# Kernel tuning notes

Hardware: AMD Instinct MI355X
Metric: run time of the kernel (lower is better)

Reference implementation:

```python
import jax, jax.numpy as jnp
from jax import lax
import numpy as np

B, DIM, HEADS, L, K = 8, 128, 8, 4096, 3
INNER = DIM * HEADS
PAD = K // 2
EPS = 1e-5
SCALE = DIM ** -0.5


def setup_inputs() -> dict:
    key = jax.random.key(0)
    ks = jax.random.split(key, 32)

    def n(i, shape, s):
        return jax.random.normal(ks[i], shape, jnp.float32) * s

    inp = {"x": jax.random.normal(ks[0], (B, DIM, L), jnp.float32)}
    inp["ln1_g"] = jnp.ones((DIM,), jnp.float32)
    inp["ln1_b"] = jnp.zeros((DIM,), jnp.float32)
    for idx, p in enumerate(("q", "k", "v")):
        base = 1 + idx * 2
        inp[p + "_dw"] = n(base, (DIM, 1, K), 0.2)        # depthwise kernel
        inp[p + "_bn_g"] = jnp.ones((DIM,), jnp.float32)
        inp[p + "_bn_b"] = jnp.zeros((DIM,), jnp.float32)
        inp[p + "_bn_m"] = jnp.zeros((DIM,), jnp.float32)  # running mean
        inp[p + "_bn_v"] = jnp.ones((DIM,), jnp.float32)   # running var
        inp[p + "_pw"] = n(base + 1, (INNER, DIM), 0.05)   # 1x1 conv dim->inner
    inp["dwc_dw"] = n(8, (DIM,), 0.2)                      # kernel-1 depthwise = per-channel scale
    inp["dwc_bn_g"] = jnp.ones((DIM,), jnp.float32)
    inp["dwc_bn_b"] = jnp.zeros((DIM,), jnp.float32)
    inp["dwc_bn_m"] = jnp.zeros((DIM,), jnp.float32)
    inp["dwc_bn_v"] = jnp.ones((DIM,), jnp.float32)
    inp["dwc_pw"] = n(9, (DIM, DIM), 0.05)
    inp["out_w"] = n(10, (DIM, INNER), 0.05)
    inp["out_b"] = jnp.zeros((DIM,), jnp.float32)
    inp["ln2_g"] = jnp.ones((DIM,), jnp.float32)
    inp["ln2_b"] = jnp.zeros((DIM,), jnp.float32)
    inp["ff_w1"] = n(11, (4 * DIM, DIM), 0.05)
    inp["ff_b1"] = jnp.zeros((4 * DIM,), jnp.float32)
    inp["ff_w2"] = n(12, (DIM, 4 * DIM), 0.05)
    inp["ff_b2"] = jnp.zeros((DIM,), jnp.float32)
    return inp


def _layernorm(x, g, b):
    # channel-wise LN over axis=1 (unbiased=False variance)
    m = jnp.mean(x, axis=1, keepdims=True)
    v = jnp.var(x, axis=1, keepdims=True)
    return (x - m) / jnp.sqrt(v + EPS) * g[None, :, None] + b[None, :, None]


def _dw_block(x, dw, g, b, m, v, pw):
    # depthwise conv (k=K, same padding) -> eval-mode BN -> 1x1 conv
    y = lax.conv_general_dilated(x, dw, (1,), [(PAD, PAD)],
                                 feature_group_count=DIM,
                                 dimension_numbers=("NCH", "OIH", "NCH"))
    y = (y - m[None, :, None]) * (g / jnp.sqrt(v + EPS))[None, :, None] + b[None, :, None]
    return jnp.einsum("oi,bil->bol", pw, y)


def reference(x, ln1_g, ln1_b,
              q_dw, q_bn_g, q_bn_b, q_bn_m, q_bn_v, q_pw,
              k_dw, k_bn_g, k_bn_b, k_bn_m, k_bn_v, k_pw,
              v_dw, v_bn_g, v_bn_b, v_bn_m, v_bn_v, v_pw,
              dwc_dw, dwc_bn_g, dwc_bn_b, dwc_bn_m, dwc_bn_v, dwc_pw,
              out_w, out_b, ln2_g, ln2_b, ff_w1, ff_b1, ff_w2, ff_b2):
    # ---- attention block (PreNorm + residual) ----
    xn = _layernorm(x, ln1_g, ln1_b)
    q = _dw_block(xn, q_dw, q_bn_g, q_bn_b, q_bn_m, q_bn_v, q_pw)  # [B, INNER, L]
    k = _dw_block(xn, k_dw, k_bn_g, k_bn_b, k_bn_m, k_bn_v, k_pw)
    v = _dw_block(xn, v_dw, v_bn_g, v_bn_b, v_bn_m, v_bn_v, v_pw)

    def split(t):  # b (h d) x -> (b h) x d
        return t.reshape(B, HEADS, DIM, L).transpose(0, 1, 3, 2).reshape(B * HEADS, L, DIM)

    q, k, v = split(q), split(k), split(v)
    k_soft = jax.nn.softmax(k, axis=-1)                       # softmax over feature dim d
    kk = jnp.einsum("nxd,nxe->nde", q, k_soft) * SCALE        # [(bh), d, d]
    # DWConv gate on q (kernel-1 depthwise -> BN -> 1x1), channels = DIM
    g_ = q * dwc_dw[None, None, :]
    g_ = (g_ - dwc_bn_m) * (dwc_bn_g / jnp.sqrt(dwc_bn_v + EPS)) + dwc_bn_b
    g_ = jnp.einsum("od,nxd->nxo", dwc_pw, g_)
    gate = jax.nn.sigmoid(g_) * v
    out = jnp.einsum("nxd,nde->nxe", v, kk) + gate            # [(bh), L, d]
    out = out.reshape(B, HEADS, L, DIM).transpose(0, 1, 3, 2).reshape(B, INNER, L)
    attn = jnp.einsum("oi,bil->bol", out_w, out) + out_b[None, :, None]
    x = attn + x

    # ---- feed-forward block (PreNorm + residual) ----
    xn = _layernorm(x, ln2_g, ln2_b)
    h = jnp.einsum("oi,bil->bol", ff_w1, xn) + ff_b1[None, :, None]
    h = jax.nn.gelu(h, approximate=False)
    h = jnp.einsum("oi,bil->bol", ff_w2, h) + ff_b2[None, :, None]
    return h + x
```

## Files before the change

kernel.cpp:

```cpp
#include <hip/hip_runtime.h>
#include <hip/hip_bf16.h>
#include <math.h>

#define DI __device__ __forceinline__

namespace {

constexpr int L = 4096;
constexpr float EPS = 1e-5f;
constexpr float SCALEF = 0.08838834764831845f;

typedef unsigned short u16;
typedef unsigned int u32;
typedef unsigned char u8;
typedef __attribute__((ext_vector_type(8))) short bf16x8;
typedef __attribute__((ext_vector_type(4))) float f32x4;

DI float b2f(u16 h){ u32 u = ((u32)h) << 16; float f; __builtin_memcpy(&f, &u, 4); return f; }
DI u16 f2b(float f){ u32 u; __builtin_memcpy(&u, &f, 4); u32 r = u + 0x7fffu + ((u >> 16) & 1u); return (u16)(r >> 16); }
DI float sigmoidf(float x){ return 1.f / (1.f + __expf(-x)); }

DI uint2 pack_fp8x8(const float* v){
  u32 lo = __builtin_amdgcn_cvt_pk_fp8_f32(v[0], v[1], 0, false);
  lo = (u32)__builtin_amdgcn_cvt_pk_fp8_f32(v[2], v[3], lo, true);
  u32 hi = __builtin_amdgcn_cvt_pk_fp8_f32(v[4], v[5], 0, false);
  hi = (u32)__builtin_amdgcn_cvt_pk_fp8_f32(v[6], v[7], hi, true);
  return make_uint2(lo, hi);
}
DI u8 f2e(float v){ return (u8)__builtin_amdgcn_cvt_pk_fp8_f32(v, v, 0, false); }
DI float e2f(u8 c){ return __builtin_amdgcn_cvt_f32_fp8((int)c, 0); }

DI int boff(int o, int d8){ return ((o >> 4) << 11) + (d8 << 7) + (((o & 15) ^ d8) << 3); }
DI int foff(int g, int k8, int nn){ return (g << 11) + (k8 << 7) + (nn << 3); }
DI int faddr(int x, int e){ return ((x >> 4) << 11) + ((e >> 3) << 7) + ((x & 15) << 3) + (e & 7); }
DI int t8off(int dhi, int nl, int x8){ return (dhi << 11) + (x8 << 7) + (((nl ^ x8 ^ dhi) & 15) << 3); }

DI void stage_a(const u16* __restrict__ g, int rs, u16* a_s, int tid){
  #pragma unroll
  for (int it = 0; it < 4; it++){
    int item = tid + 256 * it;
    int d8 = item & 15, l = item >> 4;
    *(uint4*)&a_s[l * 136 + d8 * 8] = *(const uint4*)&g[(size_t)l * rs + d8 * 8];
  }
}

__global__ __launch_bounds__(256) void ln_kernel(
    const float* __restrict__ x, const float* __restrict__ g,
    const float* __restrict__ bt, u16* __restrict__ o)
{
  const int tid = threadIdx.x;
  const int pos = blockIdx.x * 64 + (tid >> 2);
  const int part = tid & 3;
  const int b = pos >> 12, l = pos & (L - 1);
  const float* xb = x + (size_t)b * 128 * L + l;
  float vv[32];
  float s = 0.f, ss = 0.f;
  #pragma unroll
  for (int i = 0; i < 32; i++){
    float v = xb[(size_t)(part * 32 + i) * L];
    vv[i] = v; s += v; ss += v * v;
  }
  s += __shfl_xor(s, 1);  s += __shfl_xor(s, 2);
  ss += __shfl_xor(ss, 1); ss += __shfl_xor(ss, 2);
  const float m = s * (1.f / 128.f);
  const float rs = rsqrtf(ss * (1.f / 128.f) - m * m + EPS);
  #pragma unroll
  for (int c = 0; c < 4; c++){
    u16 pk[8];
    #pragma unroll
    for (int j = 0; j < 8; j++){
      int d = part * 32 + c * 8 + j;
      pk[j] = f2b((vv[c * 8 + j] - m) * rs * g[d] + bt[d]);
    }
    uint4 uu; __builtin_memcpy(&uu, pk, 16);
    *(uint4*)&o[(size_t)pos * 128 + part * 32 + c * 8] = uu;
  }
}

__global__ __launch_bounds__(256) void wpack_kernel(
    const float* __restrict__ q_pw, const float* __restrict__ k_pw,
    const float* __restrict__ v_pw, const float* __restrict__ out_w,
    const float* __restrict__ ff_w1, const float* __restrict__ ff_w2,
    const float* __restrict__ dwc_dw, const float* __restrict__ dwc_bng,
    const float* __restrict__ dwc_bnv, const float* __restrict__ dwc_bnb,
    const float* __restrict__ dwc_bnm, const float* __restrict__ dwc_pw,
    u16* __restrict__ wpk, float* __restrict__ c2, u8* __restrict__ wpk8)
{
  const int blk = blockIdx.x;
  const int tid = threadIdx.x;
  if (blk < 37){
    int t8 = blk;
    #pragma unroll
    for (int it = 0; it < 8; it++){
      int item = tid + 256 * it;
      int nn = item & 15, k8 = (item >> 4) & 15, os = item >> 8;
      int o = os * 16 + nn;
      float fv[8];
      if (t8 < 24){
        int p = t8 >> 3, h = t8 & 7;
        const float* pw = (p == 0) ? q_pw : (p == 1 ? k_pw : v_pw);
        #pragma unroll
        for (int j = 0; j < 8; j++)
          fv[j] = pw[(size_t)(h * 128 + o) * 128 + k8 * 8 + j] * 16.f;
      } else if (t8 < 32){
        #pragma unroll
        for (int j = 0; j < 8; j++)
          fv[j] = out_w[(size_t)o * 1024 + (t8 - 24) * 128 + k8 * 8 + j] * 16.f;
      } else if (t8 < 36){
        #pragma unroll
        for (int j = 0; j < 8; j++)
          fv[j] = ff_w1[(size_t)((t8 - 32) * 128 + o) * 128 + k8 * 8 + j] * 16.f;
      } else {
        #pragma unroll
        for (int j = 0; j < 8; j++){
          int d = k8 * 8 + j;
          float sD = dwc_bng[d] * rsqrtf(dwc_bnv[d] + EPS);
          fv[j] = dwc_pw[(size_t)o * 128 + d] * dwc_dw[d] * sD * 16.f;
        }
      }
      *(uint2*)&wpk8[(size_t)t8 * 16384 + foff(os, k8, nn)] = pack_fp8x8(fv);
    }
  } else if (blk < 69){
    int vitem = (blk - 37) * 256 + tid;
    int d8 = vitem & 15;
    int o  = (vitem >> 4) & 127;
    int t  = 36 + (vitem >> 11);
    const float* src = ff_w2 + (size_t)o * 512 + (t - 36) * 128 + d8 * 8;
    u16 pk[8];
    #pragma unroll
    for (int j = 0; j < 8; j++) pk[j] = f2b(src[j]);
    uint4 uu; __builtin_memcpy(&uu, pk, 16);
    *(uint4*)&wpk[(size_t)t * 16384 + boff(o, d8)] = uu;
  } else {
    int e = tid;
    if (e < 128){
      float cacc = 0.f;
      for (int d = 0; d < 128; d++){
        float sD = dwc_bng[d] * rsqrtf(dwc_bnv[d] + EPS);
        cacc += dwc_pw[(size_t)e * 128 + d] * (dwc_bnb[d] - dwc_bnm[d] * sD);
      }
      c2[e] = cacc;
    }
  }
}

struct QkvArgs {
  const float* dw[3];
  const float* bng[3];
  const float* bnb[3];
  const float* bnm[3];
  const float* bnv[3];
  u8* outp[3];
};

__global__ __launch_bounds__(256, 5) void qkv_fused_kernel(
    const u16* __restrict__ xnb, const u8* __restrict__ wpk8, QkvArgs args)
{
  __shared__ __attribute__((aligned(16))) u8 y_s8[64 * 136];
  __shared__ u16 st_s[64 * 136];
  __shared__ float4 coef[128];
  const int tid = threadIdx.x;
  const int lb = blockIdx.x;
  const int oh = blockIdx.y;
  const int bz = blockIdx.z;
  const int b  = bz / 3;
  const int p  = bz % 3;
  const int l0 = lb * 64;
  const int lane = tid & 63, wv = tid >> 6;
  const int nn = lane & 15, quad = lane >> 4;
  const int d8s = tid & 15;
  u8* w_s8 = (u8*)st_s;

  if (tid < 128){
    int d = tid;
    float sD = args.bng[p][d] * rsqrtf(args.bnv[p][d] + EPS);
    const float* dw = args.dw[p];
    coef[d] = make_float4(dw[d * 3] * sD, dw[d * 3 + 1] * sD, dw[d * 3 + 2] * sD,
                          args.bnb[p][d] - args.bnm[p][d] * sD);
  }
  __syncthreads();
  float4 cf[8];
  #pragma unroll
  for (int jj = 0; jj < 8; jj++) cf[jj] = coef[d8s * 8 + jj];
  #pragma unroll
  for (int it = 0; it < 4; it++){
    int l = (tid >> 4) + it * 16;
    int gl = l0 + l;
    const u16* rowp = xnb + ((size_t)b * L + gl) * 128 + d8s * 8;
    uint4 uc = *(const uint4*)rowp;
    uint4 um = (gl > 0)     ? *(const uint4*)(rowp - 128) : make_uint4(0, 0, 0, 0);
    uint4 up = (gl < L - 1) ? *(const uint4*)(rowp + 128) : make_uint4(0, 0, 0, 0);
    u16 em[8], ec[8], ep[8];
    __builtin_memcpy(em, &um, 16); __builtin_memcpy(ec, &uc, 16); __builtin_memcpy(ep, &up, 16);
    float fv[8];
    #pragma unroll
    for (int jj = 0; jj < 8; jj++)
      fv[jj] = cf[jj].x * b2f(em[jj]) + cf[jj].y * b2f(ec[jj]) + cf[jj].z * b2f(ep[jj]) + cf[jj].w;
    *(uint2*)&y_s8[l * 136 + d8s * 8] = pack_fp8x8(fv);
  }
  __syncthreads();
  long afq[4];
  #pragma unroll
  for (int dc = 0; dc < 4; dc++)
    afq[dc] = *(const long*)&y_s8[(wv * 16 + nn) * 136 + ((dc << 2) + quad) * 8];

  for (int hh = 0; hh < 4; hh++){
    const int h = oh * 4 + hh;
    if (hh) __syncthreads();
    const u8* src = wpk8 + ((size_t)(p * 8 + h) << 14);
    #pragma unroll
    for (int it = 0; it < 4; it++){
      int idx = (tid + 256 * it) << 4;
      *(uint4*)&w_s8[idx] = *(const uint4*)&src[idx];
    }
    __syncthreads();
    f32x4 acc[8];
    #pragma unroll
    for (int os = 0; os < 8; os++) acc[os] = (f32x4){0.f, 0.f, 0.f, 0.f};
    #pragma unroll
    for (int os = 0; os < 8; os++){
      #pragma unroll
      for (int dc = 0; dc < 4; dc++){
        int d8 = (dc << 2) + quad;
        long bf8 = *(const long*)&w_s8[foff(os, d8, nn)];
        acc[os] = __builtin_amdgcn_mfma_f32_16x16x32_fp8_fp8(afq[dc], bf8, acc[os], 0, 0, 0);
      }
    }
    #pragma unroll
    for (int os = 0; os < 8; os++)
      #pragma unroll
      for (int r = 0; r < 4; r++) acc[os][r] *= 0.0625f;
    if (p == 1){
      #pragma unroll
      for (int r = 0; r < 4; r++){
        float m = acc[0][r];
        #pragma unroll
        for (int os = 1; os < 8; os++) m = fmaxf(m, acc[os][r]);
        m = fmaxf(m, __shfl_xor(m, 1));
        m = fmaxf(m, __shfl_xor(m, 2));
        m = fmaxf(m, __shfl_xor(m, 4));
        m = fmaxf(m, __shfl_xor(m, 8));
        float s = 0.f;
        #pragma unroll
        for (int os = 0; os < 8; os++){ acc[os][r] = __expf(acc[os][r] - m); s += acc[os][r]; }
        s += __shfl_xor(s, 1);
        s += __shfl_xor(s, 2);
        s += __shfl_xor(s, 4);
        s += __shfl_xor(s, 8);
        float inv = 16.f / s;
        #pragma unroll
        for (int os = 0; os < 8; os++) acc[os][r] *= inv;
      }
    }
    __syncthreads();
    #pragma unroll
    for (int os = 0; os < 8; os++)
      #pragma unroll
      for (int r = 0; r < 4; r++)
        st_s[(wv * 16 + quad * 4 + r) * 136 + (os << 4) + nn] = f2b(acc[os][r]);
    __syncthreads();
    if (p == 2){
      u8* v8 = args.outp[2];
      size_t tbase = ((size_t)((b * 8 + h) * 64 + lb)) << 13;
      #pragma unroll
      for (int it = 0; it < 4; it++){
        int g = it, e8 = tid >> 4, n2 = tid & 15;
        const u16* sp = &st_s[(g * 16 + n2) * 136 + e8 * 8];
        float fv[8];
        #pragma unroll
        for (int j = 0; j < 8; j++) fv[j] = b2f(sp[j]);
        *(uint2*)&v8[tbase + foff(g, e8, n2)] = pack_fp8x8(fv);
      }
    } else {
      u8* outp8 = args.outp[p];
      size_t gbase = ((size_t)(b * 8 + h) * L + l0) * 128;
      #pragma unroll
      for (int it = 0; it < 4; it++){
        int item = tid + 256 * it;
        int row = item >> 4, d8 = item & 15;
        const u16* sp = &st_s[row * 136 + d8 * 8];
        float fv[8];
        #pragma unroll
        for (int j = 0; j < 8; j++) fv[j] = b2f(sp[j]);
        *(uint2*)&outp8[gbase + (size_t)row * 128 + d8 * 8] = pack_fp8x8(fv);
      }
    }
  }
}

__global__ __launch_bounds__(256, 3) void kk_kernel(
    const u8* __restrict__ qt8, const u8* __restrict__ kt8,
    float* __restrict__ kkp)
{
  __shared__ u8 qT8[16384];
  __shared__ u8 kT8[16384];
  const int tid = threadIdx.x;
  const int sp = blockIdx.x;
  const int n  = blockIdx.y;
  const int d8 = tid & 15;
  const int x8 = tid >> 4;
  const int lane = tid & 63, wv = tid >> 6;
  const int nn = lane & 15, quad = lane >> 4;
  const int m4 = (wv >> 1) << 2;
  const int e4 = (wv & 1) << 2;
  const size_t gbase = ((size_t)n * L + sp * 1024) * 128;

  uint2 rq[8], rk[8];
  #pragma unroll
  for (int j = 0; j < 8; j++){
    size_t off = gbase + (size_t)(x8 * 8 + j) * 128 + d8 * 8;
    rq[j] = *(const uint2*)&qt8[off];
    rk[j] = *(const uint2*)&kt8[off];
  }

  f32x4 acc[4][4];
  #pragma unroll
  for (int mi = 0; mi < 4; mi++)
    #pragma unroll
    for (int ei = 0; ei < 4; ei++) acc[mi][ei] = (f32x4){0.f, 0.f, 0.f, 0.f};

  for (int c = 0; c < 8; c++){
    #pragma unroll
    for (int i = 0; i < 8; i++){
      u8 cq[8], ck[8];
      #pragma unroll
      for (int j = 0; j < 8; j++){
        u8 tmp[8];
        __builtin_memcpy(tmp, &rq[j], 8); cq[j] = tmp[i];
        __builtin_memcpy(tmp, &rk[j], 8); ck[j] = tmp[i];
      }
      int d = d8 * 8 + i;
      int off = t8off(d >> 4, d & 15, x8);
      uint2 uq, uk;
      __builtin_memcpy(&uq, cq, 8); __builtin_memcpy(&uk, ck, 8);
      *(uint2*)&qT8[off] = uq;
      *(uint2*)&kT8[off] = uk;
    }
    __syncthreads();
    if (c < 7){
      #pragma unroll
      for (int j = 0; j < 8; j++){
        size_t off = gbase + (size_t)((c + 1) * 128 + x8 * 8 + j) * 128 + d8 * 8;
        rq[j] = *(const uint2*)&qt8[off];
        rk[j] = *(const uint2*)&kt8[off];
      }
    }
    #pragma unroll
    for (int ks = 0; ks < 4; ks++){
      int x8f = (ks << 2) + quad;
      long af[4], bf[4];
      #pragma unroll
      for (int t = 0; t < 4; t++){
        af[t] = *(const long*)&qT8[t8off(m4 + t, nn, x8f)];
        bf[t] = *(const long*)&kT8[t8off(e4 + t, nn, x8f)];
      }
      #pragma unroll
      for (int mi = 0; mi < 4; mi++)
        #pragma unroll
        for (int ei = 0; ei < 4; ei++)
          acc[mi][ei] = __builtin_amdgcn_mfma_f32_16x16x32_fp8_fp8(af[mi], bf[ei], acc[mi][ei], 0, 0, 0);
    }
    __syncthreads();
  }

  float* op = kkp + ((size_t)(sp * 64 + n) << 14);
  #pragma unroll
  for (int mi = 0; mi < 4; mi++){
    #pragma unroll
    for (int r = 0; r < 4; r++){
      int d = (m4 << 4) + mi * 16 + quad * 4 + r;
      #pragma unroll
      for (int ei = 0; ei < 4; ei++)
        op[d * 128 + (e4 << 4) + ei * 16 + nn] = acc[mi][ei][r];
    }
  }
}

__global__ __launch_bounds__(256) void kkred_kernel(
    const float* __restrict__ kkp, u8* __restrict__ kkbb8)
{
  int item = blockIdx.x * 256 + threadIdx.x;
  int nn = item & 15, d8 = (item >> 4) & 15, os = (item >> 8) & 7, n = item >> 11;
  int e = os * 16 + nn;
  float fv[8];
  #pragma unroll
  for (int j = 0; j < 8; j++){
    float s = 0.f;
    #pragma unroll
    for (int sp = 0; sp < 4; sp++)
      s += kkp[(size_t)sp * (64 * 16384) + n * 16384 + (d8 * 8 + j) * 128 + e];
    fv[j] = s * (SCALEF * 2.f);
  }
  *(uint2*)&kkbb8[((size_t)n << 14) + foff(os, d8, nn)] = pack_fp8x8(fv);
}

__global__ __launch_bounds__(256, 4) void gateout_kernel(
    const u8* __restrict__ qt8, const u8* __restrict__ vt8,
    const u8* __restrict__ kkbb8, const u8* __restrict__ w2tb8,
    const float* __restrict__ c2, u8* __restrict__ outt8)
{
  __shared__ __attribute__((aligned(16))) u8 q_s8[64 * 144];
  __shared__ __attribute__((aligned(16))) u8 v_s8[8192];
  const int tid = threadIdx.x;
  const int lb = blockIdx.x;
  const int n  = blockIdx.y;
  const int l0 = lb * 64;
  const int lane = tid & 63, wv = tid >> 6;
  const int nn = lane & 15, quad = lane >> 4;
  const size_t vtile = ((size_t)(n * 64 + lb)) << 13;
  const size_t qbase = ((size_t)n * L + l0) * 128;

  #pragma unroll
  for (int it = 0; it < 4; it++){
    int item = tid + 256 * it;
    int d8b = item & 15, l = item >> 4;
    *(uint2*)&q_s8[l * 144 + d8b * 8] = *(const uint2*)&qt8[qbase + (size_t)l * 128 + d8b * 8];
  }
  #pragma unroll
  for (int it = 0; it < 2; it++){
    int idx = (tid + 256 * it) << 4;
    *(uint4*)&v_s8[idx] = *(const uint4*)&vt8[vtile + idx];
  }
  __syncthreads();

  long aq[4], av[4];
  #pragma unroll
  for (int dc = 0; dc < 4; dc++){
    aq[dc] = *(const long*)&q_s8[(wv * 16 + nn) * 144 + ((dc << 2) + quad) * 8];
    av[dc] = *(const long*)&v_s8[foff(wv, (dc << 2) + quad, nn)];
  }
  const u8* kb8 = kkbb8 + ((size_t)n << 14);
  f32x4 acc_o[8], acc_g[8];
  #pragma unroll
  for (int os = 0; os < 8; os++){ acc_o[os] = (f32x4){0,0,0,0}; acc_g[os] = (f32x4){0,0,0,0}; }
  #pragma unroll
  for (int os = 0; os < 8; os++){
    #pragma unroll
    for (int dc = 0; dc < 4; dc++){
      int d8 = (dc << 2) + quad;
      long bkk = *(const long*)&kb8[foff(os, d8, nn)];
      long bw8 = *(const long*)&w2tb8[foff(os, d8, nn)];
      acc_o[os] = __builtin_amdgcn_mfma_f32_16x16x32_fp8_fp8(av[dc], bkk, acc_o[os], 0, 0, 0);
      acc_g[os] = __builtin_amdgcn_mfma_f32_16x16x32_fp8_fp8(aq[dc], bw8, acc_g[os], 0, 0, 0);
    }
  }
  __syncthreads();
  u8* st8 = q_s8;
  #pragma unroll
  for (int os = 0; os < 8; os++){
    int e = (os << 4) + nn;
    float c2v = c2[e];
    #pragma unroll
    for (int r = 0; r < 4; r++){
      int xr = wv * 16 + quad * 4 + r;
      float ve = e2f(v_s8[faddr(xr, e)]);
      float val = acc_o[os][r] * (1.f / 32.f) + sigmoidf(acc_g[os][r] * 0.0625f + c2v) * ve;
      st8[faddr(xr, e)] = f2e(val);
    }
  }
  __syncthreads();
  #pragma unroll
  for (int it = 0; it < 2; it++){
    int idx = (tid + 256 * it) << 4;
    *(uint4*)&outt8[vtile + idx] = *(const uint4*)&st8[idx];
  }
}

__global__ __launch_bounds__(256, 4) void outw_kernel(
    const u8* __restrict__ outt8, const u8* __restrict__ wpk8o,
    const float* __restrict__ out_b, const float* __restrict__ x,
    const float* __restrict__ g2, const float* __restrict__ bt2,
    float* __restrict__ x2, u8* __restrict__ xn2b8)
{
  __shared__ float stf[128 * 68];
  const int tid = threadIdx.x;
  const int lb = blockIdx.x;
  const int b  = blockIdx.y;
  const int l0 = lb * 64;
  const int lane = tid & 63, wv = tid >> 6;
  const int nn = lane & 15, quad = lane >> 4;
  f32x4 acc[8];
  #pragma unroll
  for (int os = 0; os < 8; os++) acc[os] = (f32x4){0,0,0,0};

  for (int h = 0; h < 8; h++){
    const size_t tbase = ((size_t)((b * 8 + h) * 64 + lb)) << 13;
    long af[4];
    #pragma unroll
    for (int dc = 0; dc < 4; dc++)
      af[dc] = *(const long*)&outt8[tbase + foff(wv, (dc << 2) + quad, nn)];
    const u8* bp8 = wpk8o + (h << 14);
    #pragma unroll
    for (int os = 0; os < 8; os++){
      #pragma unroll
      for (int dc = 0; dc < 4; dc++){
        long bf8 = *(const long*)&bp8[foff(os, (dc << 2) + quad, nn)];
        acc[os] = __builtin_amdgcn_mfma_f32_16x16x32_fp8_fp8(af[dc], bf8, acc[os], 0, 0, 0);
      }
    }
  }
  #pragma unroll
  for (int os = 0; os < 8; os++)
    #pragma unroll
    for (int r = 0; r < 4; r++)
      stf[((os << 4) + nn) * 68 + wv * 16 + quad * 4 + r] = acc[os][r] * 0.0625f;
  __syncthreads();
  {
    int o = tid >> 1, lh = tid & 1;
    float bias = out_b[o];
    size_t gbase = ((size_t)b * 128 + o) * L + l0 + lh * 32;
    float* sp = &stf[o * 68 + lh * 32];
    #pragma unroll
    for (int k = 0; k < 8; k++){
      float4 xv = *(const float4*)&x[gbase + k * 4];
      float4 sv = *(float4*)&sp[k * 4];
      float4 ov = make_float4(sv.x + bias + xv.x, sv.y + bias + xv.y,
                              sv.z + bias + xv.z, sv.w + bias + xv.w);
      *(float4*)&sp[k * 4] = ov;
      *(float4*)&x2[gbase + k * 4] = ov;
    }
  }
  __syncthreads();
  {
    int l = tid >> 2, part = tid & 3;
    float vv[32];
    float s = 0.f, ss = 0.f;
    #pragma unroll
    for (int i = 0; i < 32; i++){
      float v = stf[(part * 32 + i) * 68 + l];
      vv[i] = v; s += v; ss += v * v;
    }
    s += __shfl_xor(s, 1);  s += __shfl_xor(s, 2);
    ss += __shfl_xor(ss, 1); ss += __shfl_xor(ss, 2);
    float m = s * (1.f / 128.f);
    float rs = rsqrtf(ss * (1.f / 128.f) - m * m + EPS);
    #pragma unroll
    for (int c = 0; c < 4; c++){
      float fv[8];
      #pragma unroll
      for (int j = 0; j < 8; j++){
        int d = part * 32 + c * 8 + j;
        fv[j] = (vv[c * 8 + j] - m) * rs * g2[d] + bt2[d];
      }
      *(uint2*)&xn2b8[((size_t)b * L + l0 + l) * 128 + part * 32 + c * 8] = pack_fp8x8(fv);
    }
  }
}

__global__ __launch_bounds__(256, 4) void ff_fused_kernel(
    const u8* __restrict__ xn2b8, const u8* __restrict__ wpk8,
    const u16* __restrict__ wpk,
    const float* __restrict__ b1, const float* __restrict__ b2,
    const float* __restrict__ x2, float* __restrict__ outp)
{
  __shared__ __attribute__((aligned(16))) u8 a_s8[64 * 136];
  __shared__ u16 h_s[64 * 136];
  const int tid = threadIdx.x;
  const int lb = blockIdx.x;
  const int b  = blockIdx.y;
  const int l0 = lb * 64;
  const int lane = tid & 63, wv = tid >> 6;
  const int nn = lane & 15, quad = lane >> 4;

  #pragma unroll
  for (int it = 0; it < 4; it++){
    int item = tid + 256 * it;
    int d8 = item & 15, l = item >> 4;
    *(uint2*)&a_s8[l * 136 + d8 * 8] =
        *(const uint2*)&xn2b8[((size_t)b * L + l0 + l) * 128 + d8 * 8];
  }
  __syncthreads();
  long af8[4];
  #pragma unroll
  for (int dc = 0; dc < 4; dc++)
    af8[dc] = *(const long*)&a_s8[(wv * 16 + nn) * 136 + ((dc << 2) + quad) * 8];

  f32x4 acc_out[8];
  #pragma unroll
  for (int os = 0; os < 8; os++) acc_out[os] = (f32x4){0.f, 0.f, 0.f, 0.f};

  for (int fc = 0; fc < 4; fc++){
    const u8* bp1 = wpk8 + (size_t)(32 + fc) * 16384;
    f32x4 hacc[8];
    #pragma unroll
    for (int os = 0; os < 8; os++) hacc[os] = (f32x4){0.f, 0.f, 0.f, 0.f};
    #pragma unroll
    for (int os = 0; os < 8; os++){
      #pragma unroll
      for (int dc = 0; dc < 4; dc++){
        long bf8 = *(const long*)&bp1[foff(os, (dc << 2) + quad, nn)];
        hacc[os] = __builtin_amdgcn_mfma_f32_16x16x32_fp8_fp8(af8[dc], bf8, hacc[os], 0, 0, 0);
      }
    }
    __syncthreads();
    #pragma unroll
    for (int os = 0; os < 8; os++){
      float bias = b1[fc * 128 + (os << 4) + nn];
      #pragma unroll
      for (int r = 0; r < 4; r++){
        float v = hacc[os][r] * 0.0625f + bias;
        float ge = 0.5f * v * (1.f + erff(v * 0.70710678118654752f));
        h_s[(wv * 16 + quad * 4 + r) * 136 + (os << 4) + nn] = f2b(ge);
      }
    }
    __syncthreads();
    bf16x8 hf[4];
    #pragma unroll
    for (int dc = 0; dc < 4; dc++)
      hf[dc] = *(const bf16x8*)&h_s[(wv * 16 + nn) * 136 + ((dc << 2) + quad) * 8];
    const u16* bp2 = wpk + (size_t)(36 + fc) * 16384;
    #pragma unroll
    for (int os = 0; os < 8; os++){
      #pragma unroll
      for (int dc = 0; dc < 4; dc++){
        int d8 = (dc << 2) + quad;
        bf16x8 bf = *(const bf16x8*)&bp2[(os << 11) + (d8 << 7) + ((nn ^ d8) << 3)];
        acc_out[os] = __builtin_amdgcn_mfma_f32_16x16x32_bf16(hf[dc], bf, acc_out[os], 0, 0, 0);
      }
    }
  }

  float* stf = (float*)h_s;
  #pragma unroll
  for (int t = 0; t < 2; t++){
    __syncthreads();
    #pragma unroll
    for (int osl = 0; osl < 4; osl++){
      int os = t * 4 + osl;
      #pragma unroll
      for (int r = 0; r < 4; r++)
        stf[((osl << 4) + nn) * 68 + wv * 16 + quad * 4 + r] = acc_out[os][r];
    }
    __syncthreads();
    int ol = tid >> 2;
    int o  = t * 64 + ol;
    int lc = (tid & 3) * 16;
    float bias = b2[o];
    size_t gbase = ((size_t)b * 128 + o) * L + l0 + lc;
    #pragma unroll
    for (int k = 0; k < 4; k++){
      float4 sv = *(const float4*)&stf[ol * 68 + lc + k * 4];
      float4 xv = *(const float4*)&x2[gbase + k * 4];
      *(float4*)&outp[gbase + k * 4] = make_float4(sv.x + bias + xv.x, sv.y + bias + xv.y,
                                                   sv.z + bias + xv.z, sv.w + bias + xv.w);
    }
  }
}

}

extern "C" void kernel_launch(void* const* d_in, const int* in_sizes, int n_in,
                              void* d_out, int out_size, void* d_ws, size_t ws_size,
                              hipStream_t stream)
{
  const float* x      = (const float*)d_in[0];
  const float* ln1_g  = (const float*)d_in[1];
  const float* ln1_b  = (const float*)d_in[2];
  const float* q_dw   = (const float*)d_in[3];
  const float* q_bng  = (const float*)d_in[4];
  const float* q_bnb  = (const float*)d_in[5];
  const float* q_bnm  = (const float*)d_in[6];
  const float* q_bnv  = (const float*)d_in[7];
  const float* q_pw   = (const float*)d_in[8];
  const float* k_dw   = (const float*)d_in[9];
  const float* k_bng  = (const float*)d_in[10];
  const float* k_bnb  = (const float*)d_in[11];
  const float* k_bnm  = (const float*)d_in[12];
  const float* k_bnv  = (const float*)d_in[13];
  const float* k_pw   = (const float*)d_in[14];
  const float* v_dw   = (const float*)d_in[15];
  const float* v_bng  = (const float*)d_in[16];
  const float* v_bnb  = (const float*)d_in[17];
  const float* v_bnm  = (const float*)d_in[18];
  const float* v_bnv  = (const float*)d_in[19];
  const float* v_pw   = (const float*)d_in[20];
  const float* dwc_dw  = (const float*)d_in[21];
  const float* dwc_bng = (const float*)d_in[22];
  const float* dwc_bnb = (const float*)d_in[23];
  const float* dwc_bnm = (const float*)d_in[24];
  const float* dwc_bnv = (const float*)d_in[25];
  const float* dwc_pw  = (const float*)d_in[26];
  const float* out_w  = (const float*)d_in[27];
  const float* out_b  = (const float*)d_in[28];
  const float* ln2_g  = (const float*)d_in[29];
  const float* ln2_b  = (const float*)d_in[30];
  const float* ff_w1  = (const float*)d_in[31];
  const float* ff_b1  = (const float*)d_in[32];
  const float* ff_w2  = (const float*)d_in[33];
  const float* ff_b2  = (const float*)d_in[34];
  float* out = (float*)d_out;

  char* w = (char*)d_ws;
  u8*   qt8   = (u8*)(w);
  u8*   kt8   = (u8*)(w + (32ull  << 20));
  u8*   outt8 = (u8*)(w + (64ull  << 20));
  u8*   vt8   = (u8*)(w + (128ull << 20));
  u16*  xnb   = (u16*)(w + (192ull << 20));
  u8*   kkbb8 = (u8*)(w + (192ull << 20));
  u8*   xn2b8 = (u8*)(w + (192ull << 20));
  float* kkp  = (float*)(w + (200ull << 20));
  float* x2   = kkp;
  float* c2   = (float*)(w + (216ull << 20));
  u16*  wpk   = (u16*)(w + (216ull << 20) + 65536);
  u8*   wpk8  = (u8*)(w + (218ull << 20));
  u8*   wpk8o = wpk8 + ((size_t)24 << 14);
  u8*   w2tb8 = wpk8 + ((size_t)36 << 14);

  ln_kernel<<<512, 256, 0, stream>>>(x, ln1_g, ln1_b, xnb);
  wpack_kernel<<<70, 256, 0, stream>>>(q_pw, k_pw, v_pw, out_w, ff_w1, ff_w2,
                                       dwc_dw, dwc_bng, dwc_bnv, dwc_bnb, dwc_bnm, dwc_pw,
                                       wpk, c2, wpk8);

  QkvArgs qa;
  qa.dw[0] = q_dw;  qa.bng[0] = q_bng; qa.bnb[0] = q_bnb; qa.bnm[0] = q_bnm; qa.bnv[0] = q_bnv; qa.outp[0] = qt8;
  qa.dw[1] = k_dw;  qa.bng[1] = k_bng; qa.bnb[1] = k_bnb; qa.bnm[1] = k_bnm; qa.bnv[1] = k_bnv; qa.outp[1] = kt8;
  qa.dw[2] = v_dw;  qa.bng[2] = v_bng; qa.bnb[2] = v_bnb; qa.bnm[2] = v_bnm; qa.bnv[2] = v_bnv; qa.outp[2] = vt8;
  qkv_fused_kernel<<<dim3(64, 2, 24), 256, 0, stream>>>(xnb, wpk8, qa);

  kk_kernel<<<dim3(4, 64), 256, 0, stream>>>(qt8, kt8, kkp);
  kkred_kernel<<<512, 256, 0, stream>>>(kkp, kkbb8);
  gateout_kernel<<<dim3(64, 64), 256, 0, stream>>>(qt8, vt8, kkbb8, w2tb8, c2, outt8);
  outw_kernel<<<dim3(64, 8), 256, 0, stream>>>(outt8, wpk8o, out_b, x, ln2_g, ln2_b, x2, xn2b8);

  ff_fused_kernel<<<dim3(64, 8), 256, 0, stream>>>(xn2b8, wpk8, wpk, ff_b1, ff_b2, x2, out);
}
```

Baseline: 354.8 us.

## Process all heads per QKV block and stage outputs directly as fp8

The QKV kernel now loops over all 8 heads in one block instead of splitting heads across two blocks. This halves the grid and avoids recomputing the depthwise conv and LN-loaded tile twice. The output staging buffer drops from bf16 with a later fp8 repack to fp8 written straight into the reused weight buffer via f2e/faddr, and the value path is copied out with 16-byte copies. Shared memory shrinks, which may raise occupancy, but each block now runs longer over a smaller grid (1536 blocks).

```diff
diff --git a/kernel.cpp b/kernel.cpp
--- a/kernel.cpp
+++ b/kernel.cpp
@@ -157,19 +157,17 @@
     const u16* __restrict__ xnb, const u8* __restrict__ wpk8, QkvArgs args)
 {
   __shared__ __attribute__((aligned(16))) u8 y_s8[64 * 136];
-  __shared__ u16 st_s[64 * 136];
+  __shared__ __attribute__((aligned(16))) u8 w_s8[16384];
   __shared__ float4 coef[128];
   const int tid = threadIdx.x;
   const int lb = blockIdx.x;
-  const int oh = blockIdx.y;
-  const int bz = blockIdx.z;
+  const int bz = blockIdx.y;
   const int b  = bz / 3;
   const int p  = bz % 3;
   const int l0 = lb * 64;
   const int lane = tid & 63, wv = tid >> 6;
   const int nn = lane & 15, quad = lane >> 4;
   const int d8s = tid & 15;
-  u8* w_s8 = (u8*)st_s;
 
   if (tid < 128){
     int d = tid;
@@ -204,9 +202,8 @@
   for (int dc = 0; dc < 4; dc++)
     afq[dc] = *(const long*)&y_s8[(wv * 16 + nn) * 136 + ((dc << 2) + quad) * 8];
 
-  for (int hh = 0; hh < 4; hh++){
-    const int h = oh * 4 + hh;
-    if (hh) __syncthreads();
+  for (int h = 0; h < 8; h++){
+    if (h) __syncthreads();
     const u8* src = wpk8 + ((size_t)(p * 8 + h) << 14);
     #pragma unroll
     for (int it = 0; it < 4; it++){
@@ -253,23 +250,32 @@
       }
     }
     __syncthreads();
-    #pragma unroll
-    for (int os = 0; os < 8; os++)
-      #pragma unroll
-      for (int r = 0; r < 4; r++)
-        st_s[(wv * 16 + quad * 4 + r) * 136 + (os << 4) + nn] = f2b(acc[os][r]);
+    u8* st8 = w_s8;
+    if (p == 2){
+      #pragma unroll
+      for (int os = 0; os < 8; os++){
+        int e = (os << 4) + nn;
+        #pragma unroll
+        for (int r = 0; r < 4; r++)
+          st8[faddr(wv * 16 + quad * 4 + r, e)] = f2e(acc[os][r]);
+      }
+    } else {
+      #pragma unroll
+      for (int os = 0; os < 8; os++){
+        int e = (os << 4) + nn;
+        #pragma unroll
+        for (int r = 0; r < 4; r++)
+          st8[(wv * 16 + quad * 4 + r) * 136 + e] = f2e(acc[os][r]);
+      }
+    }
     __syncthreads();
     if (p == 2){
       u8* v8 = args.outp[2];
       size_t tbase = ((size_t)((b * 8 + h) * 64 + lb)) << 13;
       #pragma unroll
-      for (int it = 0; it < 4; it++){
-        int g = it, e8 = tid >> 4, n2 = tid & 15;
-        const u16* sp = &st_s[(g * 16 + n2) * 136 + e8 * 8];
-        float fv[8];
-        #pragma unroll
-        for (int j = 0; j < 8; j++) fv[j] = b2f(sp[j]);
-        *(uint2*)&v8[tbase + foff(g, e8, n2)] = pack_fp8x8(fv);
+      for (int it = 0; it < 2; it++){
+        int idx = (tid + 256 * it) << 4;
+        *(uint4*)&v8[tbase + idx] = *(const uint4*)&st8[idx];
       }
     } else {
       u8* outp8 = args.outp[p];
@@ -278,11 +284,8 @@
       for (int it = 0; it < 4; it++){
         int item = tid + 256 * it;
         int row = item >> 4, d8 = item & 15;
-        const u16* sp = &st_s[row * 136 + d8 * 8];
-        float fv[8];
-        #pragma unroll
-        for (int j = 0; j < 8; j++) fv[j] = b2f(sp[j]);
-        *(uint2*)&outp8[gbase + (size_t)row * 128 + d8 * 8] = pack_fp8x8(fv);
+        *(uint2*)&outp8[gbase + (size_t)row * 128 + d8 * 8] =
+            *(const uint2*)&st8[row * 136 + d8 * 8];
       }
     }
   }
@@ -715,7 +718,7 @@
   qa.dw[0] = q_dw;  qa.bng[0] = q_bng; qa.bnb[0] = q_bnb; qa.bnm[0] = q_bnm; qa.bnv[0] = q_bnv; qa.outp[0] = qt8;
   qa.dw[1] = k_dw;  qa.bng[1] = k_bng; qa.bnb[1] = k_bnb; qa.bnm[1] = k_bnm; qa.bnv[1] = k_bnv; qa.outp[1] = kt8;
   qa.dw[2] = v_dw;  qa.bng[2] = v_bng; qa.bnb[2] = v_bnb; qa.bnm[2] = v_bnm; qa.bnv[2] = v_bnv; qa.outp[2] = vt8;
-  qkv_fused_kernel<<<dim3(64, 2, 24), 256, 0, stream>>>(xnb, wpk8, qa);
+  qkv_fused_kernel<<<dim3(64, 24), 256, 0, stream>>>(xnb, wpk8, qa);
 
   kk_kernel<<<dim3(4, 64), 256, 0, stream>>>(qt8, kt8, kkp);
   kkred_kernel<<<512, 256, 0, stream>>>(kkp, kkbb8);
```

Result: no change. 354.7 us (-0.0%).
